# Performance work log

Hardware: AMD Instinct MI355X
Metric: run time of the kernel (lower is better)

The kernel has to match this reference:

```python
import jax, jax.numpy as jnp
import numpy as np

EMB = 256
HID = 256
NH = 8
HD = HID // NH  # 32
EPS = 1e-5


def _wn(v, g):
    # torch weight_norm(dim=0): per-output-row normalization of v
    return g[:, None] * v / jnp.linalg.norm(v, axis=1, keepdims=True)


def _ln(x, gamma, beta):
    mu = jnp.mean(x, axis=-1, keepdims=True)
    var = jnp.mean((x - mu) ** 2, axis=-1, keepdims=True)
    return (x - mu) * jax.lax.rsqrt(var + EPS) * gamma + beta


def _rope(x):
    # x: [B', S, H, D]; torchtune-style rotary embedding, base 10000
    S, D = x.shape[1], x.shape[3]
    freqs = 1.0 / (10000.0 ** (jnp.arange(0, D, 2, dtype=jnp.float32) / D))  # [D/2]
    ang = jnp.arange(S, dtype=jnp.float32)[:, None] * freqs[None, :]          # [S, D/2]
    cos = jnp.cos(ang)[None, :, None, :]
    sin = jnp.sin(ang)[None, :, None, :]
    xr = x.reshape(*x.shape[:-1], D // 2, 2)
    x0, x1 = xr[..., 0], xr[..., 1]
    out = jnp.stack([x0 * cos - x1 * sin, x1 * cos + x0 * sin], axis=-1)
    return out.reshape(x.shape)


def setup_inputs() -> dict:
    key = jax.random.key(0)
    ks = jax.random.split(key, 12)
    s = lambda shp: 0.02
    return {
        "z": jax.random.normal(ks[0], (2, 32, 512, EMB), dtype=jnp.float32),
        "ln1_g": jnp.ones((EMB,), jnp.float32),
        "ln1_b": jnp.zeros((EMB,), jnp.float32),
        "proj_v": jax.random.normal(ks[1], (3 * HID, EMB), jnp.float32) * 0.02,
        "proj_g": jnp.ones((3 * HID,), jnp.float32),
        "proj_b": jnp.zeros((3 * HID,), jnp.float32),
        "ff_v": jax.random.normal(ks[2], (EMB, HID), jnp.float32) * 0.02,
        "ff_g": jnp.ones((EMB,), jnp.float32),
        "ff_b": jnp.zeros((EMB,), jnp.float32),
        "ln2_g": jnp.ones((EMB,), jnp.float32),
        "ln2_b": jnp.zeros((EMB,), jnp.float32),
        "w1_v": jax.random.normal(ks[3], (EMB, EMB), jnp.float32) * 0.02,
        "w1_g": jnp.ones((EMB,), jnp.float32),
        "w1_b": jnp.zeros((EMB,), jnp.float32),
        "w2_v": jax.random.normal(ks[4], (EMB, EMB), jnp.float32) * 0.02,
        "w2_g": jnp.ones((EMB,), jnp.float32),
        "w2_b": jnp.zeros((EMB,), jnp.float32),
    }


def reference(z, ln1_g, ln1_b, proj_v, proj_g, proj_b, ff_v, ff_g, ff_b,
              ln2_g, ln2_b, w1_v, w1_g, w1_b, w2_v, w2_g, w2_b):
    B, U, A, E = z.shape
    BU = B * U
    Wqkv = _wn(proj_v, proj_g)   # [3H, E]
    Wo = _wn(ff_v, ff_g)         # [E, H]
    # ---- RoPE attention block ----
    z_ = _ln(z, ln1_g, ln1_b).reshape(BU, A, E)
    qkv = z_ @ Wqkv.T + proj_b                       # [BU, A, 3H]
    qkv = qkv.reshape(BU, A, NH, 3 * HD)
    q, k, v = jnp.split(qkv, 3, axis=-1)             # each [BU, A, NH, HD]
    q = _rope(q)
    k = _rope(k)
    qh = q.transpose(0, 2, 1, 3)                     # [BU, NH, A, HD]
    kh = k.transpose(0, 2, 1, 3)
    vh = v.transpose(0, 2, 1, 3)
    scores = jnp.einsum('bhqd,bhkd->bhqk', qh, kh) / jnp.sqrt(jnp.float32(HD))
    attn = jax.nn.softmax(scores, axis=-1)
    out = jnp.einsum('bhqk,bhkd->bhqd', attn, vh)    # [BU, NH, A, HD]
    out = out.transpose(0, 2, 1, 3).reshape(BU, A, HID)
    out = out @ Wo.T + ff_b
    z = z + out.reshape(B, U, A, E)
    # ---- NormFF block ----
    W1 = _wn(w1_v, w1_g)
    W2 = _wn(w2_v, w2_g)
    h = _ln(z, ln2_g, ln2_b)
    h = jax.nn.gelu(h @ W1.T + w1_b, approximate=False)
    h = h @ W2.T + w2_b
    return z + h
```

## Files before the change

kernel.cpp:

```cpp
#include <hip/hip_runtime.h>
#include <cmath>

#define EMB 256
#define NHEAD 8
#define HD 32
#define A_LEN 512
#define TOK 32768

typedef __bf16 bf16_t;
typedef __bf16 bf16x8 __attribute__((ext_vector_type(8)));
typedef __bf16 bf16x4 __attribute__((ext_vector_type(4)));
typedef float floatx4 __attribute__((ext_vector_type(4)));

#define MFMA16(a, b, c) __builtin_amdgcn_mfma_f32_16x16x32_bf16((a), (b), (c), 0, 0, 0)

__global__ __launch_bounds__(64) void setup_kernel(
    const float* __restrict__ proj_v, const float* __restrict__ proj_g,
    const float* __restrict__ ff_v, const float* __restrict__ ff_g,
    const float* __restrict__ w1_v, const float* __restrict__ w1_g,
    const float* __restrict__ w2_v, const float* __restrict__ w2_g,
    bf16_t* __restrict__ Wall, float* __restrict__ ctab,
    float* __restrict__ stab) {
    int b = blockIdx.x;
    int lane = threadIdx.x;
    if (b < 1536) {
        const float* v; const float* g; int r;
        if (b < 768)       { v = proj_v; g = proj_g; r = b; }
        else if (b < 1024) { v = ff_v;   g = ff_g;   r = b - 768; }
        else if (b < 1280) { v = w1_v;   g = w1_g;   r = b - 1024; }
        else               { v = w2_v;   g = w2_g;   r = b - 1280; }
        const floatx4* vr = (const floatx4*)(v + (size_t)r * 256);
        floatx4 x = vr[lane];
        float ss = x[0] * x[0] + x[1] * x[1] + x[2] * x[2] + x[3] * x[3];
#pragma unroll
        for (int off = 32; off >= 1; off >>= 1) ss += __shfl_xor(ss, off);
        float sc = g[r] * rsqrtf(ss);
        bf16x4 o;
        o[0] = (bf16_t)(x[0] * sc); o[1] = (bf16_t)(x[1] * sc);
        o[2] = (bf16_t)(x[2] * sc); o[3] = (bf16_t)(x[3] * sc);
        ((bf16x4*)(Wall + (size_t)b * 256))[lane] = o;
    } else {
        int idx = (b - 1536) * 64 + lane;
        int a = idx >> 4, i = idx & 15;
        float freq = expf(-(float)(2 * i) * 0.2878231366242558f);
        float ang = (float)a * freq;
        ctab[idx] = cosf(ang);
        stab[idx] = sinf(ang);
    }
}

__global__ __launch_bounds__(256, 4) void qkv_kernel(
    const float* __restrict__ z, const float* __restrict__ ln_g,
    const float* __restrict__ ln_b, const bf16_t* __restrict__ W,
    const float* __restrict__ pb, const float* __restrict__ ctab,
    const float* __restrict__ stab, bf16_t* __restrict__ qbf,
    bf16_t* __restrict__ kbf, bf16_t* __restrict__ vtb) {
    __shared__ bf16_t xns[32 * 264];
    __shared__ bf16_t stg[8704];
    int tid = threadIdx.x;
    int t0 = blockIdx.x * 32;
    int bu = t0 >> 9, a0 = t0 & 511;

#pragma unroll
    for (int it = 0; it < 2; ++it) {
        int row = it * 16 + (tid >> 4);
        int sub = tid & 15;
        const floatx4* zr = (const floatx4*)(z + (size_t)(t0 + row) * 256 + sub * 16);
        floatx4 v0 = zr[0], v1 = zr[1], v2 = zr[2], v3 = zr[3];
        float vals[16];
        ((floatx4*)vals)[0] = v0; ((floatx4*)vals)[1] = v1;
        ((floatx4*)vals)[2] = v2; ((floatx4*)vals)[3] = v3;
        float s = 0.f, q2 = 0.f;
#pragma unroll
        for (int i = 0; i < 16; ++i) { s += vals[i]; q2 += vals[i] * vals[i]; }
#pragma unroll
        for (int off = 8; off >= 1; off >>= 1) {
            s += __shfl_xor(s, off);
            q2 += __shfl_xor(q2, off);
        }
        float mu = s * (1.f / 256.f);
        float inv = rsqrtf(q2 * (1.f / 256.f) - mu * mu + 1e-5f);
        int cb = sub * 16;
        bf16x8 o0, o1;
#pragma unroll
        for (int i = 0; i < 8; ++i)
            o0[i] = (bf16_t)((vals[i] - mu) * inv * ln_g[cb + i] + ln_b[cb + i]);
#pragma unroll
        for (int i = 0; i < 8; ++i)
            o1[i] = (bf16_t)((vals[8 + i] - mu) * inv * ln_g[cb + 8 + i] + ln_b[cb + 8 + i]);
        *(bf16x8*)&xns[row * 264 + cb] = o0;
        *(bf16x8*)&xns[row * 264 + cb + 8] = o1;
    }
    __syncthreads();

    int wv = tid >> 6, lane = tid & 63, quad = lane >> 4, lidx = lane & 15;

#pragma unroll 1
    for (int sec = 0; sec < 2; ++sec) {
        bf16_t* __restrict__ dst = (sec == 0) ? qbf : kbf;
        floatx4 acc[4][2];
#pragma unroll
        for (int ntl = 0; ntl < 4; ++ntl) {
            int cb = wv * 64 + ntl * 16;
            int ht = cb >> 5;
            floatx4 b4 = *(const floatx4*)&pb[ht * 96 + sec * 32 + (cb & 31) + quad * 4];
            acc[ntl][0] = b4; acc[ntl][1] = b4;
        }
#pragma unroll 2
        for (int kc = 0; kc < 8; ++kc) {
            bf16x8 x0 = *(const bf16x8*)&xns[lidx * 264 + kc * 32 + quad * 8];
            bf16x8 x1 = *(const bf16x8*)&xns[(16 + lidx) * 264 + kc * 32 + quad * 8];
#pragma unroll
            for (int ntl = 0; ntl < 4; ++ntl) {
                int cb = wv * 64 + ntl * 16;
                int ht = cb >> 5;
                int n = ht * 96 + sec * 32 + (cb & 31) + lidx;
                bf16x8 wf = *(const bf16x8*)&W[(size_t)n * 256 + kc * 32 + quad * 8];
                acc[ntl][0] = MFMA16(wf, x0, acc[ntl][0]);
                acc[ntl][1] = MFMA16(wf, x1, acc[ntl][1]);
            }
        }
        float scl = (sec == 0) ? 0.17677669529663687f : 1.0f;
#pragma unroll
        for (int ntl = 0; ntl < 4; ++ntl) {
            int cb = wv * 64 + ntl * 16;
            int d0 = (cb & 31) + quad * 4;
            int fi = d0 >> 1;
#pragma unroll
            for (int tt = 0; tt < 2; ++tt) {
                int al = tt * 16 + lidx;
                int a = a0 + al;
                float cs0 = ctab[a * 16 + fi],     cs1 = ctab[a * 16 + fi + 1];
                float sn0 = stab[a * 16 + fi],     sn1 = stab[a * 16 + fi + 1];
                floatx4 v = acc[ntl][tt];
                bf16x4 o;
                o[0] = (bf16_t)((v[0] * cs0 - v[1] * sn0) * scl);
                o[1] = (bf16_t)((v[1] * cs0 + v[0] * sn0) * scl);
                o[2] = (bf16_t)((v[2] * cs1 - v[3] * sn1) * scl);
                o[3] = (bf16_t)((v[3] * cs1 + v[2] * sn1) * scl);
                *(bf16x4*)&stg[al * 264 + cb + quad * 4] = o;
            }
        }
        __syncthreads();
#pragma unroll
        for (int i = 0; i < 4; ++i) {
            int cid = i * 256 + tid;
            int chunk = cid & 3, al = (cid >> 2) & 31, ht = cid >> 7;
            bf16x8 vv = *(const bf16x8*)&stg[al * 264 + ht * 32 + chunk * 8];
            *(bf16x8*)&dst[((size_t)((bu * 8 + ht) * 512 + a0 + al)) * 32 + chunk * 8] = vv;
        }
        __syncthreads();
    }

    {
        floatx4 acc[4][2];
#pragma unroll
        for (int ntl = 0; ntl < 4; ++ntl) {
            int cb = wv * 64 + ntl * 16;
            int ht = cb >> 5;
            float b = pb[ht * 96 + 64 + (cb & 31) + lidx];
            acc[ntl][0] = (floatx4){b, b, b, b};
            acc[ntl][1] = (floatx4){b, b, b, b};
        }
#pragma unroll 2
        for (int kc = 0; kc < 8; ++kc) {
            bf16x8 x0 = *(const bf16x8*)&xns[lidx * 264 + kc * 32 + quad * 8];
            bf16x8 x1 = *(const bf16x8*)&xns[(16 + lidx) * 264 + kc * 32 + quad * 8];
#pragma unroll
            for (int ntl = 0; ntl < 4; ++ntl) {
                int cb = wv * 64 + ntl * 16;
                int ht = cb >> 5;
                int n = ht * 96 + 64 + (cb & 31) + lidx;
                bf16x8 wf = *(const bf16x8*)&W[(size_t)n * 256 + kc * 32 + quad * 8];
                acc[ntl][0] = MFMA16(x0, wf, acc[ntl][0]);
                acc[ntl][1] = MFMA16(x1, wf, acc[ntl][1]);
            }
        }
#pragma unroll
        for (int ntl = 0; ntl < 4; ++ntl) {
            int vcol = wv * 64 + ntl * 16 + lidx;
#pragma unroll
            for (int tt = 0; tt < 2; ++tt)
#pragma unroll
                for (int r = 0; r < 4; ++r)
                    stg[vcol * 34 + tt * 16 + quad * 4 + r] = (bf16_t)acc[ntl][tt][r];
        }
        __syncthreads();
#pragma unroll
        for (int i = 0; i < 4; ++i) {
            int cid = i * 256 + tid;
            int chunk = cid & 3, vcol = cid >> 2;
            bf16x8 vv = *(const bf16x8*)&stg[vcol * 34 + chunk * 8];
            *(bf16x8*)&vtb[((size_t)(bu * 256 + vcol)) * 512 + a0 + chunk * 8] = vv;
        }
    }
}

__global__ __launch_bounds__(512, 4) void attn_kernel(
    const bf16_t* __restrict__ qbf, const bf16_t* __restrict__ kbf,
    const bf16_t* __restrict__ vtb, bf16_t* __restrict__ ob) {
    __shared__ bf16_t Kls[512 * 32];
    __shared__ bf16_t Vt[32 * 512];
    __shared__ bf16_t Pls[8 * 16 * 64];
    int tid = threadIdx.x;
    int wv = tid >> 6, lane = tid & 63, quad = lane >> 4, lidx = lane & 15;
    int bh = blockIdx.x;
    int bu = bh >> 3, h = bh & 7;
    size_t hb = (size_t)bh * (A_LEN * HD);

#pragma unroll
    for (int i = 0; i < 4; ++i) {
        int c = tid + i * 512;
        int key = c >> 2, blk = c & 3;
        bf16x8 kv = *(const bf16x8*)&kbf[hb + (size_t)c * 8];
        *(bf16x8*)&Kls[key * 32 + ((blk ^ (key & 3)) << 3)] = kv;
        int vrow = c >> 6, vblk = c & 63;
        bf16x8 vv = *(const bf16x8*)&vtb[hb + (size_t)c * 8];
        *(bf16x8*)&Vt[vrow * 512 + ((vblk ^ (vrow & 7)) << 3)] = vv;
    }
    __syncthreads();

    int pbase = wv * (16 * 64);
    const floatx4 cm8 = (floatx4){-8.f, -8.f, -8.f, -8.f};
    const floatx4 zero4 = (floatx4){0.f, 0.f, 0.f, 0.f};

#pragma unroll 1
    for (int mt = 0; mt < 4; ++mt) {
        int q0 = wv * 64 + mt * 16;
        bf16x8 qfrag = *(const bf16x8*)&qbf[hb + (size_t)(q0 + lidx) * 32 + quad * 8];
        float l_[4] = {0.f, 0.f, 0.f, 0.f};
        floatx4 Oacc[2];
        Oacc[0] = zero4; Oacc[1] = zero4;

#pragma unroll 1
        for (int kc = 0; kc < 8; ++kc) {
            floatx4 sc[4];
#pragma unroll
            for (int t = 0; t < 4; ++t) {
                bf16x8 kf = *(const bf16x8*)&Kls[(kc * 64 + t * 16 + lidx) * 32 +
                                                 ((quad ^ (lidx & 3)) << 3)];
                sc[t] = MFMA16(qfrag, kf, cm8);
            }
            float p[4][4];
#pragma unroll
            for (int t = 0; t < 4; ++t)
#pragma unroll
                for (int r = 0; r < 4; ++r) p[t][r] = __expf(sc[t][r]);
#pragma unroll
            for (int t = 0; t < 4; ++t)
#pragma unroll
                for (int r = 0; r < 4; ++r) {
                    int row = quad * 4 + r;
                    int pc = (t * 16 + lidx) ^ ((row & 7) << 3);
                    Pls[pbase + row * 64 + pc] = (bf16_t)p[t][r];
                }
#pragma unroll
            for (int r = 0; r < 4; ++r) {
                float s = (p[0][r] + p[1][r]) + (p[2][r] + p[3][r]);
#pragma unroll
                for (int off = 8; off >= 1; off >>= 1) s += __shfl_xor(s, off);
                l_[r] += s;
            }
#pragma unroll
            for (int ks = 0; ks < 2; ++ks) {
                bf16x8 pf = *(const bf16x8*)&Pls[pbase + lidx * 64 +
                                                 (((ks * 4 + quad) ^ (lidx & 7)) << 3)];
#pragma unroll
                for (int nt = 0; nt < 2; ++nt) {
                    int vrow = nt * 16 + lidx;
                    bf16x8 vf = *(const bf16x8*)&Vt[vrow * 512 +
                        ((kc * 8 + ((ks * 4 + quad) ^ (lidx & 7))) << 3)];
                    Oacc[nt] = MFMA16(pf, vf, Oacc[nt]);
                }
            }
        }
#pragma unroll
        for (int nt = 0; nt < 2; ++nt)
#pragma unroll
            for (int r = 0; r < 4; ++r) {
                int tok = bu * 512 + q0 + quad * 4 + r;
                ob[(size_t)tok * 256 + h * 32 + nt * 16 + lidx] =
                    (bf16_t)(Oacc[nt][r] / l_[r]);
            }
    }
}

__global__ __launch_bounds__(256, 4) void tail_kernel(
    const bf16_t* __restrict__ X, const bf16_t* __restrict__ Wo,
    const float* __restrict__ obias, const float* __restrict__ zin,
    const float* __restrict__ ln_g, const float* __restrict__ ln_b,
    const bf16_t* __restrict__ W1, const float* __restrict__ b1,
    const bf16_t* __restrict__ W2, const float* __restrict__ b2,
    float* __restrict__ outp) {
    __shared__ float fbuf[32 * 264];
    __shared__ float red[32 * 8];
    __shared__ float mi[32 * 2];
    bf16_t* xbuf = (bf16_t*)fbuf;
    int tid = threadIdx.x;
    int t0 = blockIdx.x * 32;
    int wv = tid >> 6, lane = tid & 63, quad = lane >> 4, lidx = lane & 15;

    {
        int row = tid >> 3;
        int c0 = (tid & 7) * 32;
        const bf16x8* src = (const bf16x8*)&X[(size_t)(t0 + row) * 256 + c0];
        bf16x8* dst = (bf16x8*)&xbuf[row * 264 + c0];
        dst[0] = src[0]; dst[1] = src[1]; dst[2] = src[2]; dst[3] = src[3];
    }
    __syncthreads();

    float r1[4][2][4];
    {
        floatx4 acc[4][2];
#pragma unroll
        for (int i = 0; i < 4; ++i) {
            acc[i][0] = (floatx4){0.f, 0.f, 0.f, 0.f};
            acc[i][1] = (floatx4){0.f, 0.f, 0.f, 0.f};
        }
#pragma unroll 2
        for (int kc = 0; kc < 8; ++kc) {
            bf16x8 a0 = *(const bf16x8*)&xbuf[lidx * 264 + kc * 32 + quad * 8];
            bf16x8 a1 = *(const bf16x8*)&xbuf[(16 + lidx) * 264 + kc * 32 + quad * 8];
#pragma unroll
            for (int nt = 0; nt < 4; ++nt) {
                int n = wv * 64 + nt * 16 + lidx;
                bf16x8 bfr = *(const bf16x8*)&Wo[(size_t)n * 256 + kc * 32 + quad * 8];
                acc[nt][0] = MFMA16(a0, bfr, acc[nt][0]);
                acc[nt][1] = MFMA16(a1, bfr, acc[nt][1]);
            }
        }
#pragma unroll
        for (int nt = 0; nt < 4; ++nt) {
            int n = wv * 64 + nt * 16 + lidx;
            float b = obias[n];
#pragma unroll
            for (int mt = 0; mt < 2; ++mt)
#pragma unroll
                for (int r = 0; r < 4; ++r) {
                    size_t o = (size_t)(t0 + mt * 16 + quad * 4 + r) * 256 + n;
                    r1[nt][mt][r] = zin[o] + acc[nt][mt][r] + b;
                }
        }
    }

#pragma unroll
    for (int mt = 0; mt < 2; ++mt)
#pragma unroll
        for (int r = 0; r < 4; ++r) {
            float s = 0.f, ss = 0.f;
#pragma unroll
            for (int nt = 0; nt < 4; ++nt) {
                float v = r1[nt][mt][r];
                s += v; ss += v * v;
            }
#pragma unroll
            for (int off = 8; off >= 1; off >>= 1) {
                s += __shfl_xor(s, off);
                ss += __shfl_xor(ss, off);
            }
            if (lidx == 0) {
                int row = mt * 16 + quad * 4 + r;
                red[row * 8 + wv * 2] = s;
                red[row * 8 + wv * 2 + 1] = ss;
            }
        }
    __syncthreads();
    if (tid < 32) {
        float s = 0.f, ss = 0.f;
#pragma unroll
        for (int w = 0; w < 4; ++w) {
            s += red[tid * 8 + w * 2];
            ss += red[tid * 8 + w * 2 + 1];
        }
        float mu = s * (1.f / 256.f);
        mi[tid * 2] = mu;
        mi[tid * 2 + 1] = rsqrtf(ss * (1.f / 256.f) - mu * mu + 1e-5f);
    }
    __syncthreads();

    {
        float gv[4], bv[4];
#pragma unroll
        for (int nt = 0; nt < 4; ++nt) {
            int n = wv * 64 + nt * 16 + lidx;
            gv[nt] = ln_g[n]; bv[nt] = ln_b[n];
        }
#pragma unroll
        for (int mt = 0; mt < 2; ++mt)
#pragma unroll
            for (int r = 0; r < 4; ++r) {
                int row = mt * 16 + quad * 4 + r;
                float mu = mi[row * 2], inv = mi[row * 2 + 1];
#pragma unroll
                for (int nt = 0; nt < 4; ++nt) {
                    int n = wv * 64 + nt * 16 + lidx;
                    xbuf[row * 264 + n] =
                        (bf16_t)((r1[nt][mt][r] - mu) * inv * gv[nt] + bv[nt]);
                }
            }
    }
    __syncthreads();

    {
        floatx4 acc[4][2];
#pragma unroll
        for (int i = 0; i < 4; ++i) {
            acc[i][0] = (floatx4){0.f, 0.f, 0.f, 0.f};
            acc[i][1] = (floatx4){0.f, 0.f, 0.f, 0.f};
        }
#pragma unroll 2
        for (int kc = 0; kc < 8; ++kc) {
            bf16x8 a0 = *(const bf16x8*)&xbuf[lidx * 264 + kc * 32 + quad * 8];
            bf16x8 a1 = *(const bf16x8*)&xbuf[(16 + lidx) * 264 + kc * 32 + quad * 8];
#pragma unroll
            for (int nt = 0; nt < 4; ++nt) {
                int n = wv * 64 + nt * 16 + lidx;
                bf16x8 bfr = *(const bf16x8*)&W1[(size_t)n * 256 + kc * 32 + quad * 8];
                acc[nt][0] = MFMA16(a0, bfr, acc[nt][0]);
                acc[nt][1] = MFMA16(a1, bfr, acc[nt][1]);
            }
        }
        __syncthreads();
#pragma unroll
        for (int nt = 0; nt < 4; ++nt) {
            int n = wv * 64 + nt * 16 + lidx;
            float b = b1[n];
#pragma unroll
            for (int mt = 0; mt < 2; ++mt)
#pragma unroll
                for (int r = 0; r < 4; ++r) {
                    float x = acc[nt][mt][r] + b;
                    float gel = 0.5f * x * (1.f + erff(x * 0.7071067811865476f));
                    xbuf[(mt * 16 + quad * 4 + r) * 264 + n] = (bf16_t)gel;
                }
        }
    }
    __syncthreads();

    {
        floatx4 acc[4][2];
#pragma unroll
        for (int i = 0; i < 4; ++i) {
            acc[i][0] = (floatx4){0.f, 0.f, 0.f, 0.f};
            acc[i][1] = (floatx4){0.f, 0.f, 0.f, 0.f};
        }
#pragma unroll 2
        for (int kc = 0; kc < 8; ++kc) {
            bf16x8 a0 = *(const bf16x8*)&xbuf[lidx * 264 + kc * 32 + quad * 8];
            bf16x8 a1 = *(const bf16x8*)&xbuf[(16 + lidx) * 264 + kc * 32 + quad * 8];
#pragma unroll
            for (int nt = 0; nt < 4; ++nt) {
                int n = wv * 64 + nt * 16 + lidx;
                bf16x8 bfr = *(const bf16x8*)&W2[(size_t)n * 256 + kc * 32 + quad * 8];
                acc[nt][0] = MFMA16(a0, bfr, acc[nt][0]);
                acc[nt][1] = MFMA16(a1, bfr, acc[nt][1]);
            }
        }
        __syncthreads();
#pragma unroll
        for (int nt = 0; nt < 4; ++nt) {
            int n = wv * 64 + nt * 16 + lidx;
            float b = b2[n];
#pragma unroll
            for (int mt = 0; mt < 2; ++mt)
#pragma unroll
                for (int r = 0; r < 4; ++r)
                    fbuf[(mt * 16 + quad * 4 + r) * 264 + n] =
                        r1[nt][mt][r] + acc[nt][mt][r] + b;
        }
    }
    __syncthreads();

#pragma unroll
    for (int i = 0; i < 8; ++i) {
        int fid = i * 256 + tid;
        int row = fid >> 6;
        int c4 = (fid & 63) * 4;
        *(floatx4*)&outp[(size_t)(t0 + row) * 256 + c4] =
            *(const floatx4*)&fbuf[row * 264 + c4];
    }
}

extern "C" void kernel_launch(void* const* d_in, const int* in_sizes, int n_in,
                              void* d_out, int out_size, void* d_ws, size_t ws_size,
                              hipStream_t stream) {
    const float* z      = (const float*)d_in[0];
    const float* ln1_g  = (const float*)d_in[1];
    const float* ln1_b  = (const float*)d_in[2];
    const float* proj_v = (const float*)d_in[3];
    const float* proj_g = (const float*)d_in[4];
    const float* proj_b = (const float*)d_in[5];
    const float* ff_v   = (const float*)d_in[6];
    const float* ff_g   = (const float*)d_in[7];
    const float* ff_b   = (const float*)d_in[8];
    const float* ln2_g  = (const float*)d_in[9];
    const float* ln2_b  = (const float*)d_in[10];
    const float* w1_v   = (const float*)d_in[11];
    const float* w1_g   = (const float*)d_in[12];
    const float* w1_b   = (const float*)d_in[13];
    const float* w2_v   = (const float*)d_in[14];
    const float* w2_g   = (const float*)d_in[15];
    const float* w2_b   = (const float*)d_in[16];
    float* out = (float*)d_out;

    char* p = (char*)d_ws;
    bf16_t* Wall = (bf16_t*)p; p += (size_t)1536 * 256 * 2;
    float* ctab  = (float*)p;  p += 8192 * 4;
    float* stab  = (float*)p;  p += 8192 * 4;
    bf16_t* qbf  = (bf16_t*)p; p += (size_t)TOK * 256 * 2;
    bf16_t* kbf  = (bf16_t*)p; p += (size_t)TOK * 256 * 2;
    bf16_t* vtb  = (bf16_t*)p; p += (size_t)TOK * 256 * 2;
    bf16_t* abuf = (bf16_t*)p; p += (size_t)TOK * 256 * 2;

    const bf16_t* Wqkv = Wall;
    const bf16_t* Wo   = Wall + (size_t)768 * 256;
    const bf16_t* W1   = Wall + (size_t)1024 * 256;
    const bf16_t* W2   = Wall + (size_t)1280 * 256;

    setup_kernel<<<1664, 64, 0, stream>>>(proj_v, proj_g, ff_v, ff_g,
                                          w1_v, w1_g, w2_v, w2_g,
                                          Wall, ctab, stab);
    qkv_kernel<<<TOK / 32, 256, 0, stream>>>(z, ln1_g, ln1_b, Wqkv, proj_b,
                                             ctab, stab, qbf, kbf, vtb);
    attn_kernel<<<64 * 8, 512, 0, stream>>>(qbf, kbf, vtb, abuf);
    tail_kernel<<<TOK / 32, 256, 0, stream>>>(abuf, Wo, ff_b, z, ln2_g, ln2_b,
                                              W1, w1_b, W2, w2_b, out);
}
```

Measured before the change: 279.0 us.

## Interchange attention loops so K/V fragments are reused across query tiles

The attention kernel now iterates key chunks in the outer loop and the four query tiles in the inner loop. Each K and V fragment is loaded from LDS once per chunk and reused by all query tiles, and all Q fragments are preloaded before the barrier. Row-sum shuffles are deferred to the end, with the division replaced by a hardware reciprocal, and the P swizzle pattern is changed. This cuts repeated LDS reads and per-chunk cross-lane reductions, at the cost of more live registers (four sets of accumulators and row sums), which could hurt occupancy.

```diff
diff --git a/kernel.cpp b/kernel.cpp
--- a/kernel.cpp
+++ b/kernel.cpp
@@ -218,70 +218,90 @@
         bf16x8 vv = *(const bf16x8*)&vtb[hb + (size_t)c * 8];
         *(bf16x8*)&Vt[vrow * 512 + ((vblk ^ (vrow & 7)) << 3)] = vv;
     }
+    bf16x8 qf[4];
+#pragma unroll
+    for (int mt = 0; mt < 4; ++mt)
+        qf[mt] = *(const bf16x8*)&qbf[hb +
+            (size_t)(wv * 64 + mt * 16 + lidx) * 32 + quad * 8];
     __syncthreads();
 
     int pbase = wv * (16 * 64);
     const floatx4 cm8 = (floatx4){-8.f, -8.f, -8.f, -8.f};
     const floatx4 zero4 = (floatx4){0.f, 0.f, 0.f, 0.f};
+    int Sl = (lidx & 7) ^ (lidx >> 3);
+
+    floatx4 Oacc[4][2];
+    float l_[4][4];
+#pragma unroll
+    for (int mt = 0; mt < 4; ++mt) {
+        Oacc[mt][0] = zero4; Oacc[mt][1] = zero4;
+#pragma unroll
+        for (int r = 0; r < 4; ++r) l_[mt][r] = 0.f;
+    }
 
 #pragma unroll 1
+    for (int kc = 0; kc < 8; ++kc) {
+        bf16x8 kf[4];
+#pragma unroll
+        for (int t = 0; t < 4; ++t)
+            kf[t] = *(const bf16x8*)&Kls[(kc * 64 + t * 16 + lidx) * 32 +
+                                          ((quad ^ (lidx & 3)) << 3)];
+        bf16x8 vf[2][2];
+#pragma unroll
+        for (int ks = 0; ks < 2; ++ks)
+#pragma unroll
+            for (int nt = 0; nt < 2; ++nt)
+                vf[ks][nt] = *(const bf16x8*)&Vt[(nt * 16 + lidx) * 512 +
+                    ((kc * 8 + ((ks * 4 + quad) ^ (lidx & 7))) << 3)];
+
+#pragma unroll 1
+        for (int mt = 0; mt < 4; ++mt) {
+            floatx4 sc[4];
+#pragma unroll
+            for (int t = 0; t < 4; ++t)
+                sc[t] = MFMA16(qf[mt], kf[t], cm8);
+            float p[4][4];
+#pragma unroll
+            for (int t = 0; t < 4; ++t)
+#pragma unroll
+                for (int r = 0; r < 4; ++r) p[t][r] = __expf(sc[t][r]);
+#pragma unroll
+            for (int r = 0; r < 4; ++r) {
+                int row = quad * 4 + r;
+                int swz = ((quad & 1) * 4 + r) ^ (quad >> 1);
+#pragma unroll
+                for (int t = 0; t < 4; ++t) {
+                    int pc = (t * 16 + lidx) ^ (swz << 3);
+                    Pls[pbase + row * 64 + pc] = (bf16_t)p[t][r];
+                }
+                l_[mt][r] += (p[0][r] + p[1][r]) + (p[2][r] + p[3][r]);
+            }
+#pragma unroll
+            for (int ks = 0; ks < 2; ++ks) {
+                bf16x8 pf = *(const bf16x8*)&Pls[pbase + lidx * 64 +
+                                                 (((ks * 4 + quad) ^ Sl) << 3)];
+#pragma unroll
+                for (int nt = 0; nt < 2; ++nt)
+                    Oacc[mt][nt] = MFMA16(pf, vf[ks][nt], Oacc[mt][nt]);
+            }
+        }
+    }
+
+#pragma unroll
     for (int mt = 0; mt < 4; ++mt) {
         int q0 = wv * 64 + mt * 16;
-        bf16x8 qfrag = *(const bf16x8*)&qbf[hb + (size_t)(q0 + lidx) * 32 + quad * 8];
-        float l_[4] = {0.f, 0.f, 0.f, 0.f};
-        floatx4 Oacc[2];
-        Oacc[0] = zero4; Oacc[1] = zero4;
-
-#pragma unroll 1
-        for (int kc = 0; kc < 8; ++kc) {
-            floatx4 sc[4];
-#pragma unroll
-            for (int t = 0; t < 4; ++t) {
-                bf16x8 kf = *(const bf16x8*)&Kls[(kc * 64 + t * 16 + lidx) * 32 +
-                                                 ((quad ^ (lidx & 3)) << 3)];
-                sc[t] = MFMA16(qfrag, kf, cm8);
-            }
-            float p[4][4];
-#pragma unroll
-            for (int t = 0; t < 4; ++t)
-#pragma unroll
-                for (int r = 0; r < 4; ++r) p[t][r] = __expf(sc[t][r]);
-#pragma unroll
-            for (int t = 0; t < 4; ++t)
-#pragma unroll
-                for (int r = 0; r < 4; ++r) {
-                    int row = quad * 4 + r;
-                    int pc = (t * 16 + lidx) ^ ((row & 7) << 3);
-                    Pls[pbase + row * 64 + pc] = (bf16_t)p[t][r];
-                }
-#pragma unroll
-            for (int r = 0; r < 4; ++r) {
-                float s = (p[0][r] + p[1][r]) + (p[2][r] + p[3][r]);
-#pragma unroll
-                for (int off = 8; off >= 1; off >>= 1) s += __shfl_xor(s, off);
-                l_[r] += s;
-            }
-#pragma unroll
-            for (int ks = 0; ks < 2; ++ks) {
-                bf16x8 pf = *(const bf16x8*)&Pls[pbase + lidx * 64 +
-                                                 (((ks * 4 + quad) ^ (lidx & 7)) << 3)];
-#pragma unroll
-                for (int nt = 0; nt < 2; ++nt) {
-                    int vrow = nt * 16 + lidx;
-                    bf16x8 vf = *(const bf16x8*)&Vt[vrow * 512 +
-                        ((kc * 8 + ((ks * 4 + quad) ^ (lidx & 7))) << 3)];
-                    Oacc[nt] = MFMA16(pf, vf, Oacc[nt]);
-                }
-            }
-        }
-#pragma unroll
-        for (int nt = 0; nt < 2; ++nt)
-#pragma unroll
-            for (int r = 0; r < 4; ++r) {
-                int tok = bu * 512 + q0 + quad * 4 + r;
+#pragma unroll
+        for (int r = 0; r < 4; ++r) {
+            float s = l_[mt][r];
+#pragma unroll
+            for (int off = 8; off >= 1; off >>= 1) s += __shfl_xor(s, off);
+            float inv = __builtin_amdgcn_rcpf(s);
+            int tok = bu * 512 + q0 + quad * 4 + r;
+#pragma unroll
+            for (int nt = 0; nt < 2; ++nt)
                 ob[(size_t)tok * 256 + h * 32 + nt * 16 + lidx] =
-                    (bf16_t)(Oacc[nt][r] / l_[r]);
-            }
+                    (bf16_t)(Oacc[mt][nt][r] * inv);
+        }
     }
 }
 
```

Result: slower. 332.2 us (+19.1%).

## Keep attention probabilities in registers by computing transposed scores

Applied to the files above, without the earlier changes.

The score MFMA now takes K as the A operand and Q as the B operand, producing S^T. K rows are permuted so each lane's exp outputs already match the A-operand layout needed for the P·V MFMA. This removes the per-wave LDS staging buffer for P, its scattered bf16 stores and reloads, and the per-chunk 16-lane shuffle reductions of the row sums. Row sums are now accumulated per lane and reduced once per query tile with two xors and a broadcast shuffle, and the final divide becomes a reciprocal multiply. The risk is that the key permutation or operand pairing is wrong, which would give incorrect results.

```diff
diff --git a/kernel.cpp b/kernel.cpp
--- a/kernel.cpp
+++ b/kernel.cpp
@@ -201,7 +201,6 @@
     const bf16_t* __restrict__ vtb, bf16_t* __restrict__ ob) {
     __shared__ bf16_t Kls[512 * 32];
     __shared__ bf16_t Vt[32 * 512];
-    __shared__ bf16_t Pls[8 * 16 * 64];
     int tid = threadIdx.x;
     int wv = tid >> 6, lane = tid & 63, quad = lane >> 4, lidx = lane & 15;
     int bh = blockIdx.x;
@@ -220,15 +219,16 @@
     }
     __syncthreads();
 
-    int pbase = wv * (16 * 64);
     const floatx4 cm8 = (floatx4){-8.f, -8.f, -8.f, -8.f};
     const floatx4 zero4 = (floatx4){0.f, 0.f, 0.f, 0.f};
+    int krow = ((lidx >> 2) << 3) + (lidx & 3);
+    int kswz = (quad ^ (lidx & 3)) << 3;
 
 #pragma unroll 1
     for (int mt = 0; mt < 4; ++mt) {
         int q0 = wv * 64 + mt * 16;
         bf16x8 qfrag = *(const bf16x8*)&qbf[hb + (size_t)(q0 + lidx) * 32 + quad * 8];
-        float l_[4] = {0.f, 0.f, 0.f, 0.f};
+        float l_ = 0.f;
         floatx4 Oacc[2];
         Oacc[0] = zero4; Oacc[1] = zero4;
 
@@ -237,9 +237,9 @@
             floatx4 sc[4];
 #pragma unroll
             for (int t = 0; t < 4; ++t) {
-                bf16x8 kf = *(const bf16x8*)&Kls[(kc * 64 + t * 16 + lidx) * 32 +
-                                                 ((quad ^ (lidx & 3)) << 3)];
-                sc[t] = MFMA16(qfrag, kf, cm8);
+                int row = kc * 64 + (t >> 1) * 32 + ((t & 1) << 2) + krow;
+                bf16x8 kf = *(const bf16x8*)&Kls[row * 32 + kswz];
+                sc[t] = MFMA16(kf, qfrag, cm8);
             }
             float p[4][4];
 #pragma unroll
@@ -248,40 +248,39 @@
                 for (int r = 0; r < 4; ++r) p[t][r] = __expf(sc[t][r]);
 #pragma unroll
             for (int t = 0; t < 4; ++t)
-#pragma unroll
-                for (int r = 0; r < 4; ++r) {
-                    int row = quad * 4 + r;
-                    int pc = (t * 16 + lidx) ^ ((row & 7) << 3);
-                    Pls[pbase + row * 64 + pc] = (bf16_t)p[t][r];
-                }
+                l_ += (p[t][0] + p[t][1]) + (p[t][2] + p[t][3]);
+            bf16x8 pa0, pa1;
 #pragma unroll
             for (int r = 0; r < 4; ++r) {
-                float s = (p[0][r] + p[1][r]) + (p[2][r] + p[3][r]);
-#pragma unroll
-                for (int off = 8; off >= 1; off >>= 1) s += __shfl_xor(s, off);
-                l_[r] += s;
-            }
-#pragma unroll
-            for (int ks = 0; ks < 2; ++ks) {
-                bf16x8 pf = *(const bf16x8*)&Pls[pbase + lidx * 64 +
-                                                 (((ks * 4 + quad) ^ (lidx & 7)) << 3)];
-#pragma unroll
-                for (int nt = 0; nt < 2; ++nt) {
-                    int vrow = nt * 16 + lidx;
-                    bf16x8 vf = *(const bf16x8*)&Vt[vrow * 512 +
-                        ((kc * 8 + ((ks * 4 + quad) ^ (lidx & 7))) << 3)];
-                    Oacc[nt] = MFMA16(pf, vf, Oacc[nt]);
-                }
-            }
-        }
-#pragma unroll
-        for (int nt = 0; nt < 2; ++nt)
-#pragma unroll
-            for (int r = 0; r < 4; ++r) {
-                int tok = bu * 512 + q0 + quad * 4 + r;
+                pa0[r]     = (bf16_t)p[0][r];
+                pa0[4 + r] = (bf16_t)p[1][r];
+                pa1[r]     = (bf16_t)p[2][r];
+                pa1[4 + r] = (bf16_t)p[3][r];
+            }
+#pragma unroll
+            for (int nt = 0; nt < 2; ++nt) {
+                int vr = nt * 16 + lidx;
+                bf16x8 vf0 = *(const bf16x8*)&Vt[vr * 512 +
+                    ((kc * 8 + ((0 * 4 + quad) ^ (lidx & 7))) << 3)];
+                Oacc[nt] = MFMA16(pa0, vf0, Oacc[nt]);
+                bf16x8 vf1 = *(const bf16x8*)&Vt[vr * 512 +
+                    ((kc * 8 + ((1 * 4 + quad) ^ (lidx & 7))) << 3)];
+                Oacc[nt] = MFMA16(pa1, vf1, Oacc[nt]);
+            }
+        }
+
+        float s = l_;
+        s += __shfl_xor(s, 16);
+        s += __shfl_xor(s, 32);
+#pragma unroll
+        for (int r = 0; r < 4; ++r) {
+            float inv = __builtin_amdgcn_rcpf(__shfl(s, quad * 4 + r));
+            int tok = bu * 512 + q0 + quad * 4 + r;
+#pragma unroll
+            for (int nt = 0; nt < 2; ++nt)
                 ob[(size_t)tok * 256 + h * 32 + nt * 16 + lidx] =
-                    (bf16_t)(Oacc[nt][r] / l_[r]);
-            }
+                    (bf16_t)(Oacc[nt][r] * inv);
+        }
     }
 }
 
```

Result: faster. 250.6 us (-10.2%).
